# Kernel tuning notes

Hardware: AMD Instinct MI355X
Metric: run time of the kernel (lower is better)

Reference implementation:

```python
import jax, jax.numpy as jnp
import numpy as np

EMBED_DIM = 1024
NUM_HEADS = 16
HEAD_DIM = EMBED_DIM // NUM_HEADS
SCALING = HEAD_DIM ** -0.5
TGT, BSZ = 1024, 4


def setup_inputs() -> dict:
    key = jax.random.key(0)
    ks = jax.random.split(key, 8)
    query = jax.random.normal(ks[0], (TGT, BSZ, EMBED_DIM), dtype=jnp.float32)
    key_padding_mask = jax.random.randint(ks[1], (BSZ, TGT), 0, 2, dtype=jnp.int32)
    attn_mask = jax.random.normal(ks[2], (TGT, TGT), dtype=jnp.float32)
    attn_bias = jax.random.normal(ks[3], (BSZ * NUM_HEADS, TGT, TGT), dtype=jnp.float32)
    W_in = jax.random.normal(ks[4], (3 * EMBED_DIM, EMBED_DIM), dtype=jnp.float32) * 0.02
    b_in = jnp.zeros((3 * EMBED_DIM,), dtype=jnp.float32)
    W_out = jax.random.normal(ks[5], (EMBED_DIM, EMBED_DIM), dtype=jnp.float32) * 0.02
    b_out = jnp.zeros((EMBED_DIM,), dtype=jnp.float32)
    return {"query": query, "key_padding_mask": key_padding_mask,
            "attn_mask": attn_mask, "attn_bias": attn_bias,
            "W_in": W_in, "b_in": b_in, "W_out": W_out, "b_out": b_out}


def reference(query, key_padding_mask, attn_mask, attn_bias, W_in, b_in, W_out, b_out):
    tgt_len, bsz, embed_dim = query.shape
    # in_proj: (T,B,C) @ W_in.T -> (T,B,3C), chunk into q,k,v
    qkv = jnp.einsum('tbc,ec->tbe', query, W_in) + b_in
    q, k, v = jnp.split(qkv, 3, axis=-1)
    # reshape to (B*H, T, D)
    def to_bh(x):
        return x.reshape(tgt_len, bsz * NUM_HEADS, HEAD_DIM).transpose(1, 0, 2)
    q = to_bh(q) * SCALING
    k = to_bh(k)
    v = to_bh(v)
    src_len = k.shape[1]
    # scores: (B*H, T, S)
    attn_weights = jnp.einsum('ntd,nsd->nts', q, k)
    attn_weights = attn_weights + attn_mask[None, :, :]
    kpm = key_padding_mask.astype(bool)  # (B, S), True = pad
    aw = attn_weights.reshape(bsz, NUM_HEADS, tgt_len, src_len)
    aw = jnp.where(kpm[:, None, None, :], -jnp.inf, aw)
    attn_weights = aw.reshape(bsz * NUM_HEADS, tgt_len, src_len)
    attn_weights = attn_weights + attn_bias
    attn_probs = jax.nn.softmax(attn_weights, axis=-1)
    attn = jnp.einsum('nts,nsd->ntd', attn_probs, v)
    attn = attn.transpose(1, 0, 2).reshape(tgt_len, bsz, embed_dim)
    out = jnp.einsum('tbc,ec->tbe', attn, W_out) + b_out
    return out
```

## Files before the change

kernel.cpp:

```cpp
#include <hip/hip_runtime.h>

#define T_LEN 1024
#define B_SZ 4
#define EMB 1024
#define NH 16
#define HD 64
#define QKV_LD 3072

typedef _Float16 f16;
typedef __attribute__((ext_vector_type(8))) _Float16 f16x8;
typedef __attribute__((ext_vector_type(4))) _Float16 f16x4;
typedef __attribute__((ext_vector_type(4))) float f32x4;

__global__ __launch_bounds__(256) void cvt_f32_to_f16(
    const float* __restrict__ in, f16* __restrict__ out, int n4)
{
    int i = blockIdx.x * 256 + threadIdx.x;
    if (i < n4) {
        float4 v = ((const float4*)in)[i];
        f16x4 h = { (f16)v.x, (f16)v.y, (f16)v.z, (f16)v.w };
        ((f16x4*)out)[i] = h;
    }
}

template<bool OUT_HALF>
__global__ __launch_bounds__(256) void gemm_f16(
    const f16* __restrict__ A, const f16* __restrict__ B,
    const float* __restrict__ bias, void* __restrict__ Cout,
    int M, int N, int K)
{
    const int LDT = 40;
    __shared__ f16 As[128 * 40];
    __shared__ f16 Bs[128 * 40];
    const int tid = threadIdx.x;
    const int wv = tid >> 6;
    const int lane = tid & 63;
    const int lq = lane & 15, quad = lane >> 4;
    const int m0 = blockIdx.x * 128, n0 = blockIdx.y * 128;
    const int wm = (wv >> 1) * 64, wn = (wv & 1) * 64;
    const int srow = tid >> 1, soff = (tid & 1) * 16;

    f32x4 acc[4][4];
#pragma unroll
    for (int i = 0; i < 4; ++i)
#pragma unroll
        for (int j = 0; j < 4; ++j) acc[i][j] = (f32x4){0.f, 0.f, 0.f, 0.f};

    const f16* ag = A + (size_t)(m0 + srow) * K + soff;
    const f16* bg = B + (size_t)(n0 + srow) * K + soff;

    for (int k0 = 0; k0 < K; k0 += 32) {
        const f16x8 a0 = *(const f16x8*)(ag + k0);
        const f16x8 a1 = *(const f16x8*)(ag + k0 + 8);
        const f16x8 b0 = *(const f16x8*)(bg + k0);
        const f16x8 b1 = *(const f16x8*)(bg + k0 + 8);
        *(f16x8*)&As[srow * LDT + soff]     = a0;
        *(f16x8*)&As[srow * LDT + soff + 8] = a1;
        *(f16x8*)&Bs[srow * LDT + soff]     = b0;
        *(f16x8*)&Bs[srow * LDT + soff + 8] = b1;
        __syncthreads();
        f16x8 af[4], bf[4];
#pragma unroll
        for (int t = 0; t < 4; ++t) {
            af[t] = *(const f16x8*)&As[(wm + t * 16 + lq) * LDT + quad * 8];
            bf[t] = *(const f16x8*)&Bs[(wn + t * 16 + lq) * LDT + quad * 8];
        }
#pragma unroll
        for (int mt = 0; mt < 4; ++mt)
#pragma unroll
            for (int nt = 0; nt < 4; ++nt)
                acc[mt][nt] = __builtin_amdgcn_mfma_f32_16x16x32_f16(
                    af[mt], bf[nt], acc[mt][nt], 0, 0, 0);
        __syncthreads();
    }

#pragma unroll
    for (int nt = 0; nt < 4; ++nt) {
        const int col = n0 + wn + nt * 16 + lq;
        const float bb = bias[col];
#pragma unroll
        for (int mt = 0; mt < 4; ++mt) {
#pragma unroll
            for (int r = 0; r < 4; ++r) {
                const int row = m0 + wm + mt * 16 + quad * 4 + r;
                const float val = acc[mt][nt][r] + bb;
                if (OUT_HALF)
                    ((f16*)Cout)[(size_t)row * N + col] = (f16)val;
                else
                    ((float*)Cout)[(size_t)row * N + col] = val;
            }
        }
    }
}

__global__ __launch_bounds__(256) void attn_f16(
    const f16* __restrict__ qkv, const int* __restrict__ kpm,
    const float* __restrict__ attn_mask, const float* __restrict__ attn_bias,
    f16* __restrict__ ctx)
{
    const int LD = 72;
    __shared__ f16 Qs[64 * 72];
    __shared__ f16 Ks[64 * 72];
    __shared__ f16 Vs[64 * 72];
    __shared__ f16 Ps[64 * 72];

    const int tid = threadIdx.x;
    const int wv = tid >> 6;
    const int lane = tid & 63;
    const int lq = lane & 15, quad = lane >> 4;
    const int q0 = blockIdx.x * 64;
    const int bh = blockIdx.y;
    const int b = bh >> 4, hh = bh & 15;
    const size_t base = (size_t)b * QKV_LD + hh * HD;
    const int sr = tid >> 2, so = (tid & 3) * 16;

    {
        const f16* qg = qkv + (size_t)(q0 + sr) * (B_SZ * QKV_LD) + base + so;
        *(f16x8*)&Qs[sr * LD + so]     = *(const f16x8*)qg;
        *(f16x8*)&Qs[sr * LD + so + 8] = *(const f16x8*)(qg + 8);
    }

    float m_i[4], l_i[4];
    f32x4 O[4];
#pragma unroll
    for (int r = 0; r < 4; ++r) { m_i[r] = -1e30f; l_i[r] = 0.0f; }
#pragma unroll
    for (int dt = 0; dt < 4; ++dt) O[dt] = (f32x4){0.f, 0.f, 0.f, 0.f};

    for (int s0 = 0; s0 < T_LEN; s0 += 64) {
        __syncthreads();
        {
            const f16* kg = qkv + (size_t)(s0 + sr) * (B_SZ * QKV_LD) + base + EMB + so;
            *(f16x8*)&Ks[sr * LD + so]     = *(const f16x8*)kg;
            *(f16x8*)&Ks[sr * LD + so + 8] = *(const f16x8*)(kg + 8);
        }
        {
            const f16* vg = qkv + (size_t)(s0 + lane) * (B_SZ * QKV_LD) + base + 2 * EMB + wv * 16;
            const f16x8 v0 = *(const f16x8*)vg;
            const f16x8 v1 = *(const f16x8*)(vg + 8);
#pragma unroll
            for (int j = 0; j < 8; ++j) Vs[(wv * 16 + j) * LD + lane] = v0[j];
#pragma unroll
            for (int j = 0; j < 8; ++j) Vs[(wv * 16 + 8 + j) * LD + lane] = v1[j];
        }
        __syncthreads();

        f32x4 sacc[4];
#pragma unroll
        for (int nt = 0; nt < 4; ++nt) sacc[nt] = (f32x4){0.f, 0.f, 0.f, 0.f};
#pragma unroll
        for (int ks = 0; ks < 2; ++ks) {
            const f16x8 aq = *(const f16x8*)&Qs[(wv * 16 + lq) * LD + ks * 32 + quad * 8];
#pragma unroll
            for (int nt = 0; nt < 4; ++nt) {
                const f16x8 bk = *(const f16x8*)&Ks[(nt * 16 + lq) * LD + ks * 32 + quad * 8];
                sacc[nt] = __builtin_amdgcn_mfma_f32_16x16x32_f16(aq, bk, sacc[nt], 0, 0, 0);
            }
        }

        int kp[4];
#pragma unroll
        for (int nt = 0; nt < 4; ++nt) kp[nt] = kpm[b * T_LEN + s0 + nt * 16 + lq];
        float sv[4][4];
#pragma unroll
        for (int r = 0; r < 4; ++r) {
            const int t = q0 + wv * 16 + quad * 4 + r;
            const float* mrow = attn_mask + (size_t)t * T_LEN + s0;
            const float* brow = attn_bias + ((size_t)bh * T_LEN + t) * T_LEN + s0;
#pragma unroll
            for (int nt = 0; nt < 4; ++nt) {
                const float x = sacc[nt][r] * 0.125f + mrow[nt * 16 + lq] + brow[nt * 16 + lq];
                sv[r][nt] = kp[nt] ? -1e30f : x;
            }
        }

#pragma unroll
        for (int r = 0; r < 4; ++r) {
            float rm = fmaxf(fmaxf(sv[r][0], sv[r][1]), fmaxf(sv[r][2], sv[r][3]));
            rm = fmaxf(rm, __shfl_xor(rm, 1, 16));
            rm = fmaxf(rm, __shfl_xor(rm, 2, 16));
            rm = fmaxf(rm, __shfl_xor(rm, 4, 16));
            rm = fmaxf(rm, __shfl_xor(rm, 8, 16));
            const float mn = fmaxf(m_i[r], rm);
            const float alpha = __expf(m_i[r] - mn);
            m_i[r] = mn;
            float rs = 0.0f;
#pragma unroll
            for (int nt = 0; nt < 4; ++nt) {
                const float p = __expf(sv[r][nt] - mn);
                rs += p;
                Ps[(wv * 16 + quad * 4 + r) * LD + nt * 16 + lq] = (f16)p;
            }
            rs += __shfl_xor(rs, 1, 16);
            rs += __shfl_xor(rs, 2, 16);
            rs += __shfl_xor(rs, 4, 16);
            rs += __shfl_xor(rs, 8, 16);
            l_i[r] = l_i[r] * alpha + rs;
#pragma unroll
            for (int dt = 0; dt < 4; ++dt) O[dt][r] *= alpha;
        }
        __syncthreads();

#pragma unroll
        for (int ks = 0; ks < 2; ++ks) {
            const f16x8 ap = *(const f16x8*)&Ps[(wv * 16 + lq) * LD + ks * 32 + quad * 8];
#pragma unroll
            for (int dt = 0; dt < 4; ++dt) {
                const f16x8 bv = *(const f16x8*)&Vs[(dt * 16 + lq) * LD + ks * 32 + quad * 8];
                O[dt] = __builtin_amdgcn_mfma_f32_16x16x32_f16(ap, bv, O[dt], 0, 0, 0);
            }
        }
    }

#pragma unroll
    for (int r = 0; r < 4; ++r) {
        const float inv = 1.0f / l_i[r];
        const int t = q0 + wv * 16 + quad * 4 + r;
#pragma unroll
        for (int dt = 0; dt < 4; ++dt) {
            const float val = O[dt][r] * inv;
            ctx[((size_t)t * B_SZ + b) * EMB + hh * HD + dt * 16 + lq] = (f16)val;
        }
    }
}

extern "C" void kernel_launch(void* const* d_in, const int* in_sizes, int n_in,
                              void* d_out, int out_size, void* d_ws, size_t ws_size,
                              hipStream_t stream)
{
    const float* query     = (const float*)d_in[0];
    const int*   kpm       = (const int*)  d_in[1];
    const float* attn_mask = (const float*)d_in[2];
    const float* attn_bias = (const float*)d_in[3];
    const float* W_in      = (const float*)d_in[4];
    const float* b_in      = (const float*)d_in[5];
    const float* W_out     = (const float*)d_in[6];
    const float* b_out     = (const float*)d_in[7];
    float* out = (float*)d_out;

    f16* q16    = (f16*)d_ws;
    f16* win16  = q16   + (size_t)4096 * 1024;
    f16* wout16 = win16 + (size_t)3072 * 1024;
    f16* qkv16  = wout16 + (size_t)1024 * 1024;
    f16* ctx16  = qkv16 + (size_t)4096 * 3072;

    cvt_f32_to_f16<<<4096 * 1024 / 1024, 256, 0, stream>>>(query, q16,   4096 * 1024 / 4);
    cvt_f32_to_f16<<<3072 * 1024 / 1024, 256, 0, stream>>>(W_in,  win16, 3072 * 1024 / 4);
    cvt_f32_to_f16<<<1024 * 1024 / 1024, 256, 0, stream>>>(W_out, wout16,1024 * 1024 / 4);

    dim3 g1(4096 / 128, 3072 / 128);
    gemm_f16<true><<<g1, 256, 0, stream>>>(q16, win16, b_in, qkv16, 4096, 3072, 1024);

    dim3 g2(T_LEN / 64, B_SZ * NH);
    attn_f16<<<g2, 256, 0, stream>>>(qkv16, kpm, attn_mask, attn_bias, ctx16);

    dim3 g3(4096 / 128, 1024 / 128);
    gemm_f16<false><<<g3, 256, 0, stream>>>(ctx16, wout16, b_out, out, 4096, 1024, 1024);
}
```

Baseline: 606.1 us.

## Write head-major Q/K and transposed V from GEMM, stream K/V from global in attention

The QKV projection epilogue now scatters results into head-major Q and K buffers and a transposed V buffer, so attention can read MFMA fragments directly from global memory without LDS staging or block-wide barriers. Attention computes S^T (K as A operand) so each lane owns one query row, loads mask, bias and padding as vectorized float4/int4 per lane, and uses only wave-local barriers around a per-wave P tile. The GEMM also switches to global_load_lds direct-to-LDS copies with an unpadded tile. The costs are a scattered, uncoalesced epilogue for the transposed V, possible LDS bank conflicts from the unpadded GEMM tile, and K/V reads that depend on cache reuse instead of shared memory.

Result: faster. 591.2 us (-2.5%).

```diff
diff --git a/kernel.cpp b/kernel.cpp
--- a/kernel.cpp
+++ b/kernel.cpp
@@ -5,12 +5,17 @@
 #define EMB 1024
 #define NH 16
 #define HD 64
-#define QKV_LD 3072
 
 typedef _Float16 f16;
 typedef __attribute__((ext_vector_type(8))) _Float16 f16x8;
 typedef __attribute__((ext_vector_type(4))) _Float16 f16x4;
 typedef __attribute__((ext_vector_type(4))) float f32x4;
+
+__device__ __forceinline__ void gload16(const f16* g, f16* l) {
+    __builtin_amdgcn_global_load_lds(
+        (const __attribute__((address_space(1))) void*)g,
+        (__attribute__((address_space(3))) void*)l, 16, 0, 0);
+}
 
 __global__ __launch_bounds__(256) void cvt_f32_to_f16(
     const float* __restrict__ in, f16* __restrict__ out, int n4)
@@ -23,22 +28,28 @@
     }
 }
 
-template<bool OUT_HALF>
-__global__ __launch_bounds__(256) void gemm_f16(
+template<int MODE>
+__global__ __launch_bounds__(256) void gemm_f16_v2(
     const f16* __restrict__ A, const f16* __restrict__ B,
-    const float* __restrict__ bias, void* __restrict__ Cout,
+    const float* __restrict__ bias, float* __restrict__ outF,
+    f16* __restrict__ Qh, f16* __restrict__ Kh, f16* __restrict__ Vth,
     int M, int N, int K)
 {
-    const int LDT = 40;
-    __shared__ f16 As[128 * 40];
-    __shared__ f16 Bs[128 * 40];
+    __shared__ f16 As[128 * 32];
+    __shared__ f16 Bs[128 * 32];
     const int tid = threadIdx.x;
-    const int wv = tid >> 6;
-    const int lane = tid & 63;
+    const int wv = tid >> 6, lane = tid & 63;
     const int lq = lane & 15, quad = lane >> 4;
     const int m0 = blockIdx.x * 128, n0 = blockIdx.y * 128;
     const int wm = (wv >> 1) * 64, wn = (wv & 1) * 64;
-    const int srow = tid >> 1, soff = (tid & 1) * 16;
+
+    const int s1 = tid, s2 = 256 + tid;
+    const f16* a1 = A + (size_t)(m0 + (s1 >> 2)) * K + (s1 & 3) * 8;
+    const f16* a2 = A + (size_t)(m0 + (s2 >> 2)) * K + (s2 & 3) * 8;
+    const f16* b1 = B + (size_t)(n0 + (s1 >> 2)) * K + (s1 & 3) * 8;
+    const f16* b2 = B + (size_t)(n0 + (s2 >> 2)) * K + (s2 & 3) * 8;
+    f16* lA1 = As + s1 * 8; f16* lA2 = As + s2 * 8;
+    f16* lB1 = Bs + s1 * 8; f16* lB2 = Bs + s2 * 8;
 
     f32x4 acc[4][4];
 #pragma unroll
@@ -46,24 +57,18 @@
 #pragma unroll
         for (int j = 0; j < 4; ++j) acc[i][j] = (f32x4){0.f, 0.f, 0.f, 0.f};
 
-    const f16* ag = A + (size_t)(m0 + srow) * K + soff;
-    const f16* bg = B + (size_t)(n0 + srow) * K + soff;
-
     for (int k0 = 0; k0 < K; k0 += 32) {
-        const f16x8 a0 = *(const f16x8*)(ag + k0);
-        const f16x8 a1 = *(const f16x8*)(ag + k0 + 8);
-        const f16x8 b0 = *(const f16x8*)(bg + k0);
-        const f16x8 b1 = *(const f16x8*)(bg + k0 + 8);
-        *(f16x8*)&As[srow * LDT + soff]     = a0;
-        *(f16x8*)&As[srow * LDT + soff + 8] = a1;
-        *(f16x8*)&Bs[srow * LDT + soff]     = b0;
-        *(f16x8*)&Bs[srow * LDT + soff + 8] = b1;
+        __syncthreads();
+        gload16(a1 + k0, lA1);
+        gload16(a2 + k0, lA2);
+        gload16(b1 + k0, lB1);
+        gload16(b2 + k0, lB2);
         __syncthreads();
         f16x8 af[4], bf[4];
 #pragma unroll
         for (int t = 0; t < 4; ++t) {
-            af[t] = *(const f16x8*)&As[(wm + t * 16 + lq) * LDT + quad * 8];
-            bf[t] = *(const f16x8*)&Bs[(wn + t * 16 + lq) * LDT + quad * 8];
+            af[t] = *(const f16x8*)&As[(wm + t * 16 + lq) * 32 + quad * 8];
+            bf[t] = *(const f16x8*)&Bs[(wn + t * 16 + lq) * 32 + quad * 8];
         }
 #pragma unroll
         for (int mt = 0; mt < 4; ++mt)
@@ -71,156 +76,163 @@
             for (int nt = 0; nt < 4; ++nt)
                 acc[mt][nt] = __builtin_amdgcn_mfma_f32_16x16x32_f16(
                     af[mt], bf[nt], acc[mt][nt], 0, 0, 0);
-        __syncthreads();
     }
 
 #pragma unroll
     for (int nt = 0; nt < 4; ++nt) {
         const int col = n0 + wn + nt * 16 + lq;
         const float bb = bias[col];
-#pragma unroll
-        for (int mt = 0; mt < 4; ++mt) {
-#pragma unroll
-            for (int r = 0; r < 4; ++r) {
-                const int row = m0 + wm + mt * 16 + quad * 4 + r;
-                const float val = acc[mt][nt][r] + bb;
-                if (OUT_HALF)
-                    ((f16*)Cout)[(size_t)row * N + col] = (f16)val;
-                else
-                    ((float*)Cout)[(size_t)row * N + col] = val;
-            }
-        }
-    }
-}
-
-__global__ __launch_bounds__(256) void attn_f16(
-    const f16* __restrict__ qkv, const int* __restrict__ kpm,
+        if (MODE == 0) {
+#pragma unroll
+            for (int mt = 0; mt < 4; ++mt)
+#pragma unroll
+                for (int r = 0; r < 4; ++r) {
+                    const int row = m0 + wm + mt * 16 + quad * 4 + r;
+                    outF[(size_t)row * N + col] = acc[mt][nt][r] + bb;
+                }
+        } else {
+            const int sec = col >> 10, cc = col & 1023;
+            const int h = cc >> 6, d = cc & 63;
+#pragma unroll
+            for (int mt = 0; mt < 4; ++mt)
+#pragma unroll
+                for (int r = 0; r < 4; ++r) {
+                    const int row = m0 + wm + mt * 16 + quad * 4 + r;
+                    const int t = row >> 2, b = row & 3;
+                    const int bh = b * NH + h;
+                    const f16 v = (f16)(acc[mt][nt][r] + bb);
+                    if (sec == 0)      Qh[(size_t)bh * 65536 + t * 64 + d] = v;
+                    else if (sec == 1) Kh[(size_t)bh * 65536 + t * 64 + d] = v;
+                    else               Vth[(size_t)bh * 65536 + d * 1024 + t] = v;
+                }
+        }
+    }
+}
+
+__global__ __launch_bounds__(256) void attn_v2(
+    const f16* __restrict__ Qh, const f16* __restrict__ Kh,
+    const f16* __restrict__ Vth, const int* __restrict__ kpm,
     const float* __restrict__ attn_mask, const float* __restrict__ attn_bias,
     f16* __restrict__ ctx)
 {
-    const int LD = 72;
-    __shared__ f16 Qs[64 * 72];
-    __shared__ f16 Ks[64 * 72];
-    __shared__ f16 Vs[64 * 72];
-    __shared__ f16 Ps[64 * 72];
+    const int LDP = 72;
+    __shared__ f16 Ps[4 * 16 * LDP];
 
     const int tid = threadIdx.x;
-    const int wv = tid >> 6;
-    const int lane = tid & 63;
+    const int wv = tid >> 6, lane = tid & 63;
     const int lq = lane & 15, quad = lane >> 4;
     const int q0 = blockIdx.x * 64;
     const int bh = blockIdx.y;
     const int b = bh >> 4, hh = bh & 15;
-    const size_t base = (size_t)b * QKV_LD + hh * HD;
-    const int sr = tid >> 2, so = (tid & 3) * 16;
-
-    {
-        const f16* qg = qkv + (size_t)(q0 + sr) * (B_SZ * QKV_LD) + base + so;
-        *(f16x8*)&Qs[sr * LD + so]     = *(const f16x8*)qg;
-        *(f16x8*)&Qs[sr * LD + so + 8] = *(const f16x8*)(qg + 8);
-    }
-
-    float m_i[4], l_i[4];
+
+    const f16* Qb = Qh + (size_t)bh * 65536;
+    const f16* Kb = Kh + (size_t)bh * 65536;
+    const f16* Vb = Vth + (size_t)bh * 65536;
+    f16* Pw = Ps + wv * 16 * LDP;
+
+    const int t = q0 + wv * 16 + lq;
+    const float* mrow = attn_mask + (size_t)t * T_LEN;
+    const float* brow = attn_bias + ((size_t)bh * T_LEN + t) * T_LEN;
+    const int* kpr = kpm + b * T_LEN;
+
+    f16x8 bq[2];
+    bq[0] = *(const f16x8*)(Qb + (size_t)t * 64 + quad * 8);
+    bq[1] = *(const f16x8*)(Qb + (size_t)t * 64 + 32 + quad * 8);
+
+    float m_i = -1e30f, l_i = 0.0f;
     f32x4 O[4];
 #pragma unroll
-    for (int r = 0; r < 4; ++r) { m_i[r] = -1e30f; l_i[r] = 0.0f; }
-#pragma unroll
     for (int dt = 0; dt < 4; ++dt) O[dt] = (f32x4){0.f, 0.f, 0.f, 0.f};
 
     for (int s0 = 0; s0 < T_LEN; s0 += 64) {
-        __syncthreads();
-        {
-            const f16* kg = qkv + (size_t)(s0 + sr) * (B_SZ * QKV_LD) + base + EMB + so;
-            *(f16x8*)&Ks[sr * LD + so]     = *(const f16x8*)kg;
-            *(f16x8*)&Ks[sr * LD + so + 8] = *(const f16x8*)(kg + 8);
-        }
-        {
-            const f16* vg = qkv + (size_t)(s0 + lane) * (B_SZ * QKV_LD) + base + 2 * EMB + wv * 16;
-            const f16x8 v0 = *(const f16x8*)vg;
-            const f16x8 v1 = *(const f16x8*)(vg + 8);
-#pragma unroll
-            for (int j = 0; j < 8; ++j) Vs[(wv * 16 + j) * LD + lane] = v0[j];
-#pragma unroll
-            for (int j = 0; j < 8; ++j) Vs[(wv * 16 + 8 + j) * LD + lane] = v1[j];
-        }
-        __syncthreads();
-
         f32x4 sacc[4];
 #pragma unroll
-        for (int nt = 0; nt < 4; ++nt) sacc[nt] = (f32x4){0.f, 0.f, 0.f, 0.f};
+        for (int st = 0; st < 4; ++st) sacc[st] = (f32x4){0.f, 0.f, 0.f, 0.f};
+#pragma unroll
+        for (int ks = 0; ks < 2; ++ks)
+#pragma unroll
+            for (int st = 0; st < 4; ++st) {
+                const f16x8 ak = *(const f16x8*)(Kb + (size_t)(s0 + st * 16 + lq) * 64 + ks * 32 + quad * 8);
+                sacc[st] = __builtin_amdgcn_mfma_f32_16x16x32_f16(ak, bq[ks], sacc[st], 0, 0, 0);
+            }
+
+        float4 m4[4], b4[4]; int4 kp4[4];
+#pragma unroll
+        for (int st = 0; st < 4; ++st) {
+            const int sb = s0 + st * 16 + quad * 4;
+            m4[st] = *(const float4*)(mrow + sb);
+            b4[st] = *(const float4*)(brow + sb);
+            kp4[st] = *(const int4*)(kpr + sb);
+        }
+
+        float sv[4][4];
+        float rm = -1e30f;
+#pragma unroll
+        for (int st = 0; st < 4; ++st) {
+            const float mv[4] = {m4[st].x, m4[st].y, m4[st].z, m4[st].w};
+            const float bv[4] = {b4[st].x, b4[st].y, b4[st].z, b4[st].w};
+            const int kv[4] = {kp4[st].x, kp4[st].y, kp4[st].z, kp4[st].w};
+#pragma unroll
+            for (int r = 0; r < 4; ++r) {
+                const float x = sacc[st][r] * 0.125f + mv[r] + bv[r];
+                sv[st][r] = kv[r] ? -1e30f : x;
+                rm = fmaxf(rm, sv[st][r]);
+            }
+        }
+        rm = fmaxf(rm, __shfl_xor(rm, 16));
+        rm = fmaxf(rm, __shfl_xor(rm, 32));
+        const float mn = fmaxf(m_i, rm);
+        const float alpha = __expf(m_i - mn);
+        m_i = mn;
+
+        __builtin_amdgcn_wave_barrier();
+        float rs = 0.0f;
+#pragma unroll
+        for (int st = 0; st < 4; ++st) {
+            f16x4 pv;
+#pragma unroll
+            for (int r = 0; r < 4; ++r) {
+                const float p = __expf(sv[st][r] - mn);
+                rs += p;
+                pv[r] = (f16)p;
+            }
+            *(f16x4*)&Pw[lq * LDP + st * 16 + quad * 4] = pv;
+        }
+        rs += __shfl_xor(rs, 16);
+        rs += __shfl_xor(rs, 32);
+        l_i = l_i * alpha + rs;
+
+        float aB[4];
+#pragma unroll
+        for (int r = 0; r < 4; ++r) aB[r] = __shfl(alpha, quad * 4 + r, 16);
+#pragma unroll
+        for (int dt = 0; dt < 4; ++dt)
+#pragma unroll
+            for (int r = 0; r < 4; ++r) O[dt][r] *= aB[r];
+
+        __builtin_amdgcn_wave_barrier();
+
 #pragma unroll
         for (int ks = 0; ks < 2; ++ks) {
-            const f16x8 aq = *(const f16x8*)&Qs[(wv * 16 + lq) * LD + ks * 32 + quad * 8];
-#pragma unroll
-            for (int nt = 0; nt < 4; ++nt) {
-                const f16x8 bk = *(const f16x8*)&Ks[(nt * 16 + lq) * LD + ks * 32 + quad * 8];
-                sacc[nt] = __builtin_amdgcn_mfma_f32_16x16x32_f16(aq, bk, sacc[nt], 0, 0, 0);
-            }
-        }
-
-        int kp[4];
-#pragma unroll
-        for (int nt = 0; nt < 4; ++nt) kp[nt] = kpm[b * T_LEN + s0 + nt * 16 + lq];
-        float sv[4][4];
-#pragma unroll
-        for (int r = 0; r < 4; ++r) {
-            const int t = q0 + wv * 16 + quad * 4 + r;
-            const float* mrow = attn_mask + (size_t)t * T_LEN + s0;
-            const float* brow = attn_bias + ((size_t)bh * T_LEN + t) * T_LEN + s0;
-#pragma unroll
-            for (int nt = 0; nt < 4; ++nt) {
-                const float x = sacc[nt][r] * 0.125f + mrow[nt * 16 + lq] + brow[nt * 16 + lq];
-                sv[r][nt] = kp[nt] ? -1e30f : x;
-            }
-        }
-
-#pragma unroll
-        for (int r = 0; r < 4; ++r) {
-            float rm = fmaxf(fmaxf(sv[r][0], sv[r][1]), fmaxf(sv[r][2], sv[r][3]));
-            rm = fmaxf(rm, __shfl_xor(rm, 1, 16));
-            rm = fmaxf(rm, __shfl_xor(rm, 2, 16));
-            rm = fmaxf(rm, __shfl_xor(rm, 4, 16));
-            rm = fmaxf(rm, __shfl_xor(rm, 8, 16));
-            const float mn = fmaxf(m_i[r], rm);
-            const float alpha = __expf(m_i[r] - mn);
-            m_i[r] = mn;
-            float rs = 0.0f;
-#pragma unroll
-            for (int nt = 0; nt < 4; ++nt) {
-                const float p = __expf(sv[r][nt] - mn);
-                rs += p;
-                Ps[(wv * 16 + quad * 4 + r) * LD + nt * 16 + lq] = (f16)p;
-            }
-            rs += __shfl_xor(rs, 1, 16);
-            rs += __shfl_xor(rs, 2, 16);
-            rs += __shfl_xor(rs, 4, 16);
-            rs += __shfl_xor(rs, 8, 16);
-            l_i[r] = l_i[r] * alpha + rs;
-#pragma unroll
-            for (int dt = 0; dt < 4; ++dt) O[dt][r] *= alpha;
-        }
-        __syncthreads();
-
-#pragma unroll
-        for (int ks = 0; ks < 2; ++ks) {
-            const f16x8 ap = *(const f16x8*)&Ps[(wv * 16 + lq) * LD + ks * 32 + quad * 8];
+            const f16x8 ap = *(const f16x8*)&Pw[lq * LDP + ks * 32 + quad * 8];
 #pragma unroll
             for (int dt = 0; dt < 4; ++dt) {
-                const f16x8 bv = *(const f16x8*)&Vs[(dt * 16 + lq) * LD + ks * 32 + quad * 8];
-                O[dt] = __builtin_amdgcn_mfma_f32_16x16x32_f16(ap, bv, O[dt], 0, 0, 0);
-            }
-        }
-    }
-
+                const f16x8 av = *(const f16x8*)(Vb + (size_t)(dt * 16 + lq) * 1024 + s0 + ks * 32 + quad * 8);
+                O[dt] = __builtin_amdgcn_mfma_f32_16x16x32_f16(ap, av, O[dt], 0, 0, 0);
+            }
+        }
+    }
+
+    float lB[4];
+#pragma unroll
+    for (int r = 0; r < 4; ++r) lB[r] = __shfl(l_i, quad * 4 + r, 16);
 #pragma unroll
     for (int r = 0; r < 4; ++r) {
-        const float inv = 1.0f / l_i[r];
-        const int t = q0 + wv * 16 + quad * 4 + r;
-#pragma unroll
-        for (int dt = 0; dt < 4; ++dt) {
-            const float val = O[dt][r] * inv;
-            ctx[((size_t)t * B_SZ + b) * EMB + hh * HD + dt * 16 + lq] = (f16)val;
-        }
+        const float inv = 1.0f / lB[r];
+        const int tt = q0 + wv * 16 + quad * 4 + r;
+#pragma unroll
+        for (int dt = 0; dt < 4; ++dt)
+            ctx[((size_t)tt * B_SZ + b) * EMB + hh * HD + dt * 16 + lq] = (f16)(O[dt][r] * inv);
     }
 }
 
@@ -239,21 +251,25 @@
     float* out = (float*)d_out;
 
     f16* q16    = (f16*)d_ws;
-    f16* win16  = q16   + (size_t)4096 * 1024;
-    f16* wout16 = win16 + (size_t)3072 * 1024;
-    f16* qkv16  = wout16 + (size_t)1024 * 1024;
-    f16* ctx16  = qkv16 + (size_t)4096 * 3072;
-
-    cvt_f32_to_f16<<<4096 * 1024 / 1024, 256, 0, stream>>>(query, q16,   4096 * 1024 / 4);
-    cvt_f32_to_f16<<<3072 * 1024 / 1024, 256, 0, stream>>>(W_in,  win16, 3072 * 1024 / 4);
-    cvt_f32_to_f16<<<1024 * 1024 / 1024, 256, 0, stream>>>(W_out, wout16,1024 * 1024 / 4);
+    f16* win16  = q16    + (size_t)4096 * 1024;
+    f16* wout16 = win16  + (size_t)3072 * 1024;
+    f16* Qh     = wout16 + (size_t)1024 * 1024;
+    f16* Kh     = Qh     + (size_t)64 * 65536;
+    f16* Vth    = Kh     + (size_t)64 * 65536;
+    f16* ctx16  = Vth    + (size_t)64 * 65536;
+
+    cvt_f32_to_f16<<<4096 * 1024 / 1024, 256, 0, stream>>>(query, q16,    4096 * 1024 / 4);
+    cvt_f32_to_f16<<<3072 * 1024 / 1024, 256, 0, stream>>>(W_in,  win16,  3072 * 1024 / 4);
+    cvt_f32_to_f16<<<1024 * 1024 / 1024, 256, 0, stream>>>(W_out, wout16, 1024 * 1024 / 4);
 
     dim3 g1(4096 / 128, 3072 / 128);
-    gemm_f16<true><<<g1, 256, 0, stream>>>(q16, win16, b_in, qkv16, 4096, 3072, 1024);
+    gemm_f16_v2<2><<<g1, 256, 0, stream>>>(q16, win16, b_in, nullptr,
+                                           Qh, Kh, Vth, 4096, 3072, 1024);
 
     dim3 g2(T_LEN / 64, B_SZ * NH);
-    attn_f16<<<g2, 256, 0, stream>>>(qkv16, kpm, attn_mask, attn_bias, ctx16);
+    attn_v2<<<g2, 256, 0, stream>>>(Qh, Kh, Vth, kpm, attn_mask, attn_bias, ctx16);
 
     dim3 g3(4096 / 128, 1024 / 128);
-    gemm_f16<false><<<g3, 256, 0, stream>>>(ctx16, wout16, b_out, out, 4096, 1024, 1024);
-}
+    gemm_f16_v2<0><<<g3, 256, 0, stream>>>(ctx16, wout16, b_out, out,
+                                           nullptr, nullptr, nullptr, 4096, 1024, 1024);
+}
```
